# Kernel optimization log

Measured on AMD Instinct MI355X. Metric: run time of the kernel, lower is better.

The kernel has to match this reference:

```python
import jax, jax.numpy as jnp
import numpy as np

NUM_EXPERTS_PER_TOK = 8

def setup_inputs() -> dict:
    key = jax.random.key(0)
    kx, kw = jax.random.split(key)
    x = jax.random.normal(kx, (4, 8192, 2048), dtype=jnp.float32)
    kernel_DE = jax.random.normal(kw, (2048, 64), dtype=jnp.float32) * 0.02
    return {"x": x, "kernel_DE": kernel_DE}

def reference(x, kernel_DE):
    # router logits: [B,S,D] @ [D,E] -> [B,S,E]
    logits_BSE = jnp.einsum('BSD,DE->BSE', x, kernel_DE)
    # full softmax over experts in fp32
    gating_BSE = jax.nn.softmax(logits_BSE.astype(jnp.float32), axis=-1)
    # top-k expert selection
    weights_BSK, selected_experts_BSK = jax.lax.top_k(gating_BSE, NUM_EXPERTS_PER_TOK)
    # renormalize the selected weights with a second softmax (cast to cfg.dtype=float32)
    normalized_weights_BSK = jax.nn.softmax(weights_BSK.astype(jnp.float32), axis=-1)
    return normalized_weights_BSK, selected_experts_BSK
```

## Files before the change

### kernel.cpp

```cpp
#include <hip/hip_runtime.h>
#include <math.h>

#define NTOK   32768
#define DDIM   2048
#define NEXP   64
#define TOKB   64
#define BLOCK  512
#define NTI    2
#define RD     128
#define NR     (DDIM / RD)
#define JB     (RD / 16)
#define BUFSZ  (RD * NEXP)

union Smem {
    float wbuf[2 * BUFSZ];
    float logit[TOKB][NEXP + 1];
};

#define XGET(v, dd) ((dd)==0 ? (v).x : (dd)==1 ? (v).y : (dd)==2 ? (v).z : (v).w)

#define GLD16(gp, lp) __builtin_amdgcn_global_load_lds(                      \
    (const __attribute__((address_space(1))) void*)(gp),                     \
    (__attribute__((address_space(3))) void*)(lp), 16, 0, 0)

#define RBAR() {                                             \
    asm volatile("s_waitcnt lgkmcnt(0)" ::: "memory");       \
    asm volatile("s_waitcnt vmcnt(8)" ::: "memory");         \
    __builtin_amdgcn_s_barrier();                            \
    asm volatile("" ::: "memory"); }

#define STEP(p, XP, PFX) {                                                   \
    float4 wc[4];                                                            \
    _Pragma("unroll")                                                        \
    for (int dd = 0; dd < 4; ++dd)                                           \
        wc[dd] = *(const float4*)(wj + ((p) * 4 + dd) * NEXP);               \
    _Pragma("unroll")                                                        \
    for (int dd = 0; dd < 4; ++dd) {                                         \
        _Pragma("unroll")                                                    \
        for (int i = 0; i < NTI; ++i) {                                      \
            const float xv = XGET(XP[i], dd);                                \
            a2[i][0] = fmaf(xv, wc[dd].x, a2[i][0]);                         \
            a2[i][1] = fmaf(xv, wc[dd].y, a2[i][1]);                         \
            a2[i][2] = fmaf(xv, wc[dd].z, a2[i][2]);                         \
            a2[i][3] = fmaf(xv, wc[dd].w, a2[i][3]);                         \
        }                                                                    \
    }                                                                        \
    if (PFX) {                                                               \
        XP[0] = *(const float4*)(xa + (p) * 4 + 16);                         \
        XP[1] = *(const float4*)(xb + (p) * 4 + 16);                         \
    } }

__global__ __launch_bounds__(BLOCK, 2)
void router_kernel(const float* __restrict__ x, const float* __restrict__ wde,
                   float* __restrict__ out) {
    __shared__ Smem sm;
    float* smw = sm.wbuf;

    const int tid  = threadIdx.x;
    const int lane = tid & 63;
    const int w    = tid >> 6;
    const int g    = lane >> 4;
    const int el   = lane & 15;
    const int tl0  = w * 8 + g * NTI;
    const int tok0 = blockIdx.x * TOKB;

    auto stage = [&](int r, int bofs) {
        const char* gsrc = (const char*)wde + (size_t)r * (RD * NEXP * 4);
        char* lbase = (char*)(smw + bofs);
        #pragma unroll
        for (int s = 0; s < 4; ++s) {
            const int c = s * 8 + w;
            GLD16(gsrc + c * 1024 + lane * 16, lbase + c * 1024);
        }
    };

    float a2[NTI][4], s01[NTI][4], s23[NTI][4];
    #pragma unroll
    for (int i = 0; i < NTI; ++i)
        #pragma unroll
        for (int e = 0; e < 4; ++e) { a2[i][e] = 0.0f; s01[i][e] = 0.0f; s23[i][e] = 0.0f; }

    stage(0, 0);
    __builtin_amdgcn_sched_barrier(0);

    const float* xq = x + (size_t)(tok0 + tl0) * DDIM;
    float4 X0[NTI], X1[NTI], X2[NTI], X3[NTI];
    #pragma unroll
    for (int i = 0; i < NTI; ++i) {
        const float* xi = xq + (size_t)i * DDIM;
        X0[i] = *(const float4*)(xi + 0);
        X1[i] = *(const float4*)(xi + 4);
        X2[i] = *(const float4*)(xi + 8);
        X3[i] = *(const float4*)(xi + 12);
    }
    RBAR();

    int bo = 0;
    for (int r = 0; r < NR; ++r) {
        const bool lastr = (r == NR - 1);
        if (!lastr) {
            stage(r + 1, bo ^ BUFSZ);
            __builtin_amdgcn_sched_barrier(0);
        }
        const float* wl = smw + bo + el * 4;
        #pragma unroll
        for (int jb = 0; jb < JB; ++jb) {
            const float* wj = wl + jb * 16 * NEXP;
            const float* xa = xq + jb * 16;
            const float* xb = xa + DDIM;
            const bool pf = (jb < JB - 1) || !lastr;
            STEP(0, X0, pf)
            STEP(1, X1, pf)
            STEP(2, X2, pf)
            STEP(3, X3, pf)
        }
        RBAR();
        bo ^= BUFSZ;
        xq += RD;
        if ((r & 3) == 3) {
            const int q = r >> 2;
            #pragma unroll
            for (int i = 0; i < NTI; ++i)
                #pragma unroll
                for (int e = 0; e < 4; ++e) {
                    if (q == 0)      s01[i][e]  = a2[i][e];
                    else if (q == 1) s01[i][e] += a2[i][e];
                    else if (q == 2) s23[i][e]  = a2[i][e];
                    else             s23[i][e] += a2[i][e];
                    a2[i][e] = 0.0f;
                }
        }
    }

    #pragma unroll
    for (int i = 0; i < NTI; ++i)
        #pragma unroll
        for (int e = 0; e < 4; ++e)
            sm.logit[tl0 + i][el * 4 + e] = s01[i][e] + s23[i][e];
    __syncthreads();

    if (tid < 64) {
        const int tok = tok0 + tid;
        float lg[NEXP];
        #pragma unroll
        for (int e = 0; e < NEXP; ++e) lg[e] = sm.logit[tid][e];

        float m = lg[0];
        #pragma unroll
        for (int e = 1; e < NEXP; ++e) m = fmaxf(m, lg[e]);
        float s = 0.0f;
        #pragma unroll
        for (int e = 0; e < NEXP; ++e) { lg[e] = expf(lg[e] - m); s += lg[e]; }

        unsigned long long chosen = 0ull;
        float wv[8], wi[8];
        #pragma unroll
        for (int k = 0; k < 8; ++k) {
            float best = -1.0f; int bi = 0;
            #pragma unroll
            for (int e = 0; e < NEXP; ++e) {
                bool ok = (((chosen >> e) & 1ull) == 0ull) && (lg[e] > best);
                best = ok ? lg[e] : best;
                bi   = ok ? e : bi;
            }
            chosen |= (1ull << bi);
            wv[k] = best;
            wi[k] = (float)bi;
        }

        float p0 = wv[0] / s;
        float e2[8]; float s2 = 0.0f;
        #pragma unroll
        for (int k = 0; k < 8; ++k) { e2[k] = expf(wv[k] / s - p0); s2 += e2[k]; }

        float4* ow = (float4*)(out + (size_t)tok * 8);
        ow[0] = make_float4(e2[0]/s2, e2[1]/s2, e2[2]/s2, e2[3]/s2);
        ow[1] = make_float4(e2[4]/s2, e2[5]/s2, e2[6]/s2, e2[7]/s2);
        float4* oi = (float4*)(out + (size_t)NTOK * 8 + (size_t)tok * 8);
        oi[0] = make_float4(wi[0], wi[1], wi[2], wi[3]);
        oi[1] = make_float4(wi[4], wi[5], wi[6], wi[7]);
    }
}

extern "C" void kernel_launch(void* const* d_in, const int* in_sizes, int n_in,
                              void* d_out, int out_size, void* d_ws, size_t ws_size,
                              hipStream_t stream) {
    const float* x   = (const float*)d_in[0];
    const float* wde = (const float*)d_in[1];
    float* out       = (float*)d_out;
    router_kernel<<<dim3(NTOK / TOKB), dim3(BLOCK), 0, stream>>>(x, wde, out);
}
```

Measured before the change: 512.2 us.

## Stage x tiles into LDS via async global_load_lds with XOR swizzle

```diff
diff --git a/kernel.cpp b/kernel.cpp
--- a/kernel.cpp
+++ b/kernel.cpp
@@ -7,13 +7,13 @@
 #define TOKB   64
 #define BLOCK  512
 #define NTI    2
-#define RD     128
+#define RD     64
 #define NR     (DDIM / RD)
 #define JB     (RD / 16)
-#define BUFSZ  (RD * NEXP)
+#define CHF    (RD * NEXP)
 
 union Smem {
-    float wbuf[2 * BUFSZ];
+    float buf[4 * CHF];
     float logit[TOKB][NEXP + 1];
 };
 
@@ -25,36 +25,37 @@
 
 #define RBAR() {                                             \
     asm volatile("s_waitcnt lgkmcnt(0)" ::: "memory");       \
-    asm volatile("s_waitcnt vmcnt(8)" ::: "memory");         \
+    asm volatile("s_waitcnt vmcnt(0)" ::: "memory");         \
     __builtin_amdgcn_s_barrier();                            \
     asm volatile("" ::: "memory"); }
 
-#define STEP(p, XP, PFX) {                                                   \
-    float4 wc[4];                                                            \
-    _Pragma("unroll")                                                        \
-    for (int dd = 0; dd < 4; ++dd)                                           \
-        wc[dd] = *(const float4*)(wj + ((p) * 4 + dd) * NEXP);               \
+#define STEP(p) {                                                            \
+    float4 wc0 = *(const float4*)(wj + ((p) * 4 + 0) * NEXP);                \
+    float4 wc1 = *(const float4*)(wj + ((p) * 4 + 1) * NEXP);                \
+    float4 wc2 = *(const float4*)(wj + ((p) * 4 + 2) * NEXP);                \
+    float4 wc3 = *(const float4*)(wj + ((p) * 4 + 3) * NEXP);                \
+    float4 xq0 = *(const float4*)(xj0 + (((p) ^ g) << 2));                   \
+    float4 xq1 = *(const float4*)(xj1 + (((p) ^ g) << 2));                   \
     _Pragma("unroll")                                                        \
     for (int dd = 0; dd < 4; ++dd) {                                         \
-        _Pragma("unroll")                                                    \
-        for (int i = 0; i < NTI; ++i) {                                      \
-            const float xv = XGET(XP[i], dd);                                \
-            a2[i][0] = fmaf(xv, wc[dd].x, a2[i][0]);                         \
-            a2[i][1] = fmaf(xv, wc[dd].y, a2[i][1]);                         \
-            a2[i][2] = fmaf(xv, wc[dd].z, a2[i][2]);                         \
-            a2[i][3] = fmaf(xv, wc[dd].w, a2[i][3]);                         \
-        }                                                                    \
-    }                                                                        \
-    if (PFX) {                                                               \
-        XP[0] = *(const float4*)(xa + (p) * 4 + 16);                         \
-        XP[1] = *(const float4*)(xb + (p) * 4 + 16);                         \
+        const float4 wcd = (dd==0) ? wc0 : (dd==1) ? wc1 : (dd==2) ? wc2 : wc3; \
+        {   const float xv = XGET(xq0, dd);                                  \
+            a2[0][0] = fmaf(xv, wcd.x, a2[0][0]);                            \
+            a2[0][1] = fmaf(xv, wcd.y, a2[0][1]);                            \
+            a2[0][2] = fmaf(xv, wcd.z, a2[0][2]);                            \
+            a2[0][3] = fmaf(xv, wcd.w, a2[0][3]); }                          \
+        {   const float xv = XGET(xq1, dd);                                  \
+            a2[1][0] = fmaf(xv, wcd.x, a2[1][0]);                            \
+            a2[1][1] = fmaf(xv, wcd.y, a2[1][1]);                            \
+            a2[1][2] = fmaf(xv, wcd.z, a2[1][2]);                            \
+            a2[1][3] = fmaf(xv, wcd.w, a2[1][3]); }                          \
     } }
 
 __global__ __launch_bounds__(BLOCK, 2)
 void router_kernel(const float* __restrict__ x, const float* __restrict__ wde,
                    float* __restrict__ out) {
     __shared__ Smem sm;
-    float* smw = sm.wbuf;
+    float* smw = sm.buf;
 
     const int tid  = threadIdx.x;
     const int lane = tid & 63;
@@ -64,13 +65,21 @@
     const int tl0  = w * 8 + g * NTI;
     const int tok0 = blockIdx.x * TOKB;
 
-    auto stage = [&](int r, int bofs) {
-        const char* gsrc = (const char*)wde + (size_t)r * (RD * NEXP * 4);
-        char* lbase = (char*)(smw + bofs);
+    const int   k     = (2 * w + (lane >> 5)) & 3;
+    const char* xsrc0 = (const char*)x
+        + ((size_t)(tok0 + (lane >> 4)) * DDIM) * 4
+        + (size_t)((((lane & 15) ^ k)) * 16);
+
+    auto stage = [&](int r, int bo2) {
+        const char* gw = (const char*)wde + (size_t)r * (CHF * 4);
+        char* lw = (char*)(smw + bo2);
+        char* lx = (char*)(smw + 2 * CHF + bo2);
         #pragma unroll
-        for (int s = 0; s < 4; ++s) {
-            const int c = s * 8 + w;
-            GLD16(gsrc + c * 1024 + lane * 16, lbase + c * 1024);
+        for (int s = 0; s < 2; ++s) {
+            const int c = w + 8 * s;
+            GLD16(gw + c * 1024 + lane * 16, lw + c * 1024);
+            GLD16(xsrc0 + (size_t)c * (4 * DDIM * 4) + (size_t)r * (RD * 4),
+                  lx + c * 1024);
         }
     };
 
@@ -82,43 +91,30 @@
 
     stage(0, 0);
     __builtin_amdgcn_sched_barrier(0);
-
-    const float* xq = x + (size_t)(tok0 + tl0) * DDIM;
-    float4 X0[NTI], X1[NTI], X2[NTI], X3[NTI];
-    #pragma unroll
-    for (int i = 0; i < NTI; ++i) {
-        const float* xi = xq + (size_t)i * DDIM;
-        X0[i] = *(const float4*)(xi + 0);
-        X1[i] = *(const float4*)(xi + 4);
-        X2[i] = *(const float4*)(xi + 8);
-        X3[i] = *(const float4*)(xi + 12);
-    }
     RBAR();
 
     int bo = 0;
     for (int r = 0; r < NR; ++r) {
-        const bool lastr = (r == NR - 1);
-        if (!lastr) {
-            stage(r + 1, bo ^ BUFSZ);
+        if (r + 1 < NR) {
+            stage(r + 1, bo ^ CHF);
             __builtin_amdgcn_sched_barrier(0);
         }
-        const float* wl = smw + bo + el * 4;
+        const float* wl  = smw + bo + el * 4;
+        const float* xt0 = smw + 2 * CHF + bo + (w * 8 + g * NTI) * RD;
         #pragma unroll
         for (int jb = 0; jb < JB; ++jb) {
-            const float* wj = wl + jb * 16 * NEXP;
-            const float* xa = xq + jb * 16;
-            const float* xb = xa + DDIM;
-            const bool pf = (jb < JB - 1) || !lastr;
-            STEP(0, X0, pf)
-            STEP(1, X1, pf)
-            STEP(2, X2, pf)
-            STEP(3, X3, pf)
+            const float* wj  = wl + jb * 16 * NEXP;
+            const float* xj0 = xt0 + jb * 16;
+            const float* xj1 = xt0 + RD + jb * 16;
+            STEP(0)
+            STEP(1)
+            STEP(2)
+            STEP(3)
         }
         RBAR();
-        bo ^= BUFSZ;
-        xq += RD;
-        if ((r & 3) == 3) {
-            const int q = r >> 2;
+        bo ^= CHF;
+        if ((r & 7) == 7) {
+            const int q = r >> 3;
             #pragma unroll
             for (int i = 0; i < NTI; ++i)
                 #pragma unroll
@@ -155,7 +151,7 @@
         unsigned long long chosen = 0ull;
         float wv[8], wi[8];
         #pragma unroll
-        for (int k = 0; k < 8; ++k) {
+        for (int kk = 0; kk < 8; ++kk) {
             float best = -1.0f; int bi = 0;
             #pragma unroll
             for (int e = 0; e < NEXP; ++e) {
@@ -164,14 +160,14 @@
                 bi   = ok ? e : bi;
             }
             chosen |= (1ull << bi);
-            wv[k] = best;
-            wi[k] = (float)bi;
+            wv[kk] = best;
+            wi[kk] = (float)bi;
         }
 
         float p0 = wv[0] / s;
         float e2[8]; float s2 = 0.0f;
         #pragma unroll
-        for (int k = 0; k < 8; ++k) { e2[k] = expf(wv[k] / s - p0); s2 += e2[k]; }
+        for (int kk = 0; kk < 8; ++kk) { e2[kk] = expf(wv[kk] / s - p0); s2 += e2[kk]; }
 
         float4* ow = (float4*)(out + (size_t)tok * 8);
         ow[0] = make_float4(e2[0]/s2, e2[1]/s2, e2[2]/s2, e2[3]/s2);
```

New measurement: 416.1 us. -18.8%, faster.
